# Kernel tuning notes

Measured on AMD Instinct MI355X. Metric: run time of the kernel, lower is better.

Reference implementation:

```python
import jax, jax.numpy as jnp
import numpy as np

B, S, D, H, RANK, NC = 2, 2048, 1024, 16, 128, 16
DH = D // H


def setup_inputs() -> dict:
    key = jax.random.key(0)
    ks = jax.random.split(key, 10)
    x = jax.random.normal(ks[0], (B, S, D), jnp.float32)
    # causal mask, broadcast over batch and heads like torch's [B,1,S,S]
    mask = jnp.tril(jnp.ones((S, S), dtype=bool))[None, None]
    # orthogonal-ish init approximated by scaled gaussian
    compress_neurons = jax.random.normal(ks[1], (NC, D, RANK), jnp.float32) / np.sqrt(D)
    router_Q = jax.random.normal(ks[2], (NC, D), jnp.float32) * 0.02
    router_K = jax.random.normal(ks[3], (NC, D), jnp.float32) * 0.02
    router_V = jax.random.normal(ks[4], (NC, D), jnp.float32) * 0.02
    wQ = jax.random.normal(ks[5], (D, RANK), jnp.float32) / np.sqrt(RANK)
    wK = jax.random.normal(ks[6], (D, RANK), jnp.float32) / np.sqrt(RANK)
    wV = jax.random.normal(ks[7], (D, RANK), jnp.float32) / np.sqrt(RANK)
    wO = jax.random.normal(ks[8], (D, D), jnp.float32) / np.sqrt(D)
    return {"x": x, "mask": mask, "compress_neurons": compress_neurons,
            "router_Q": router_Q, "router_K": router_K, "router_V": router_V,
            "wQ": wQ, "wK": wK, "wV": wV, "wO": wO}


def reference(x, mask, compress_neurons, router_Q, router_K, router_V, wQ, wK, wV, wO):
    def compress(router_w):
        # router scores -> softmax over all n_compress neurons
        w = jax.nn.softmax(jnp.einsum('bsd,nd->bsn', x, router_w), axis=-1)  # [B,S,NC]
        # softmax-weighted sum of all neuron projections (fused einsum)
        return jnp.einsum('bsd,ndr,bsn->bsr', x, compress_neurons, w)  # [B,S,RANK]

    hQ = compress(router_Q)
    hK = compress(router_K)
    hV = compress(router_V)
    # expand rank -> d_model (Linear weight [D,RANK]), then split heads
    Q = jnp.einsum('bsr,dr->bsd', hQ, wQ).reshape(B, S, H, DH).transpose(0, 2, 1, 3)
    K = jnp.einsum('bsr,dr->bsd', hK, wK).reshape(B, S, H, DH).transpose(0, 2, 1, 3)
    V = jnp.einsum('bsr,dr->bsd', hV, wV).reshape(B, S, H, DH).transpose(0, 2, 1, 3)
    scores = jnp.einsum('bhqd,bhkd->bhqk', Q, K) / np.sqrt(DH)  # [B,H,S,S]
    scores = jnp.where(mask, scores, -jnp.inf)
    attn = jax.nn.softmax(scores, axis=-1)
    attn_out = jnp.einsum('bhqk,bhkd->bhqd', attn, V)
    attn_out = attn_out.transpose(0, 2, 1, 3).reshape(B, S, D)
    # dropout omitted (eval mode / dropout=0)
    return jnp.einsum('bsd,ed->bse', attn_out, wO)
```

## Files before the change

kernel.cpp:

```cpp
#include <hip/hip_runtime.h>
#include <hip/hip_bf16.h>
#include <math.h>

#define B_ 2
#define S_ 2048
#define D_ 1024
#define H_ 16
#define RANK_ 128
#define NC_ 16
#define DH_ 64
#define T_ (B_*S_)
#define NZ_ 2176

typedef __attribute__((ext_vector_type(8))) __bf16 bf16x8;
typedef __attribute__((ext_vector_type(8))) unsigned short u16x8;
typedef __attribute__((ext_vector_type(4))) unsigned short u16x4;
typedef __attribute__((ext_vector_type(4))) float f32x4;
typedef __attribute__((ext_vector_type(16))) float f32x16;

#if __has_builtin(__builtin_amdgcn_exp2f)
#define EXP2F(x) __builtin_amdgcn_exp2f(x)
#else
#define EXP2F(x) exp2f(x)
#endif

__device__ __forceinline__ unsigned short f2bu(float f) {
    __hip_bfloat16 h = __float2bfloat16(f);
    unsigned short u; __builtin_memcpy(&u, &h, 2); return u;
}
__device__ __forceinline__ float bu2f(unsigned short u) {
    __hip_bfloat16 h; __builtin_memcpy(&h, &u, 2); return __bfloat162float(h);
}

__device__ __forceinline__ void gl_lds16(const unsigned short* g, unsigned short* l) {
    __builtin_amdgcn_global_load_lds(
        (const __attribute__((address_space(1))) void*)g,
        (__attribute__((address_space(3))) void*)l, 16, 0, 0);
}

__device__ __forceinline__ unsigned cvtpk_bf16(float lo, float hi) {
    unsigned r;
    asm("v_cvt_pk_bf16_f32 %0, %1, %2" : "=v"(r) : "v"(lo), "v"(hi));
    return r;
}
__device__ __forceinline__ void plswap(unsigned &a, unsigned &b) {
    asm("v_permlane32_swap_b32 %0, %1" : "+v"(a), "+v"(b));
}

__device__ __forceinline__ bool sniff_f32(const unsigned* __restrict__ p) {
    int votes = 0;
    #pragma unroll
    for (int i = 0; i < 64; i++) {
        unsigned e = (p[i] >> 23) & 0xFFu;
        votes += (e >= 0x60u && e <= 0x8Fu) ? 1 : 0;
    }
    return votes >= 32;
}

struct Cvt { const void* src[9]; unsigned short* dst[9]; const void* C; unsigned short* Ct; };

__global__ __launch_bounds__(256) void k_inputs(Cvt cv,
    const unsigned* __restrict__ probe)
{
    bool f32 = sniff_f32(probe);
    if (blockIdx.x < 512) {
        int bid = blockIdx.x;
        int d0 = (bid & 15) * 64, r0 = ((bid >> 4) & 1) * 64, n = bid >> 5;
        __shared__ unsigned short tile[64][65];
        for (int idx = threadIdx.x; idx < 4096; idx += 256) {
            int row = idx >> 6, col = idx & 63;
            size_t si = ((size_t)n*D_ + d0 + row)*RANK_ + r0 + col;
            tile[row][col] = f32 ? f2bu(((const float*)cv.C)[si])
                                 : ((const unsigned short*)cv.C)[si];
        }
        __syncthreads();
        for (int idx = threadIdx.x; idx < 4096; idx += 256) {
            int row = idx >> 6, col = idx & 63;
            cv.Ct[((size_t)(n*RANK_ + r0 + row))*D_ + d0 + col] = tile[col][row];
        }
        return;
    }
    const int offs[9] = {0, 4194304, 4210688, 4227072, 4243456,
                         4259840, 4390912, 4521984, 4653056};
    const int total4 = 5701632 / 4;
    int nconv = gridDim.x - 512;
    int stride = nconv * 256;
    for (int g = (blockIdx.x - 512) * 256 + threadIdx.x; g < total4; g += stride) {
        int i = g * 4;
        int seg = 0;
        #pragma unroll
        for (int s = 1; s < 9; s++) seg += (i >= offs[s]) ? 1 : 0;
        int local = i - offs[seg];
        const void* sp = cv.src[seg];
        u16x4 v = {0, 0, 0, 0};
        if (sp) {
            if (f32) {
                f32x4 x = *(const f32x4*)((const float*)sp + local);
                #pragma unroll
                for (int j = 0; j < 4; j++) v[j] = f2bu(x[j]);
            } else {
                v = *(const u16x4*)((const unsigned short*)sp + local);
            }
        }
        *(u16x4*)(cv.dst[seg] + local) = v;
    }
}

template<int MT, int MODE>
__global__ __launch_bounds__(256) void k_mfma_gemm(const unsigned short* __restrict__ A,
    const unsigned short* __restrict__ Bm, void* __restrict__ Cout,
    const unsigned* __restrict__ probe, int M, int N, int K)
{
    bool f32out = false;
    if (MODE == 2) f32out = sniff_f32(probe);
    __shared__ __align__(16) unsigned short As[MT*32*32];
    __shared__ __align__(16) unsigned short Bs[128*32];
    const int tid = threadIdx.x;
    const int wv = tid >> 6, lane = tid & 63;
    const int wm = (wv >> 1) * (MT*16), wn = (wv & 1) * 64;
    const int quad = lane >> 4, l16 = lane & 15;
    const int m0 = blockIdx.x * (MT*32), n0 = blockIdx.y * 128;

    const f32x4 z4 = {0.f, 0.f, 0.f, 0.f};
    f32x4 acc[MT][4];
    #pragma unroll
    for (int i = 0; i < MT; i++)
        #pragma unroll
        for (int j = 0; j < 4; j++) acc[i][j] = z4;

    for (int k0 = 0; k0 < K; k0 += 32) {
        __syncthreads();
        #pragma unroll
        for (int c = 0; c < MT/2; c++) {
            int idx = wv*64 + c*256 + lane;
            gl_lds16(A + (size_t)(m0 + (idx >> 2))*K + k0 + (idx & 3)*8,
                     &As[(wv*64 + c*256)*8]);
        }
        #pragma unroll
        for (int c = 0; c < 2; c++) {
            int idx = wv*64 + c*256 + lane;
            gl_lds16(Bm + (size_t)(n0 + (idx >> 2))*K + k0 + (idx & 3)*8,
                     &Bs[(wv*64 + c*256)*8]);
        }
        __syncthreads();
        bf16x8 af[MT], bfr[4];
        #pragma unroll
        for (int mt = 0; mt < MT; mt++) af[mt]  = *(const bf16x8*)&As[(wm + mt*16 + l16)*32 + quad*8];
        #pragma unroll
        for (int nt = 0; nt < 4; nt++) bfr[nt] = *(const bf16x8*)&Bs[(wn + nt*16 + l16)*32 + quad*8];
        #pragma unroll
        for (int mt = 0; mt < MT; mt++)
            #pragma unroll
            for (int nt = 0; nt < 4; nt++)
                acc[mt][nt] = __builtin_amdgcn_mfma_f32_16x16x32_bf16(af[mt], bfr[nt], acc[mt][nt], 0, 0, 0);
    }
    #pragma unroll
    for (int mt = 0; mt < MT; mt++)
        #pragma unroll
        for (int nt = 0; nt < 4; nt++) {
            int col = n0 + wn + nt*16 + l16;
            #pragma unroll
            for (int r = 0; r < 4; r++) {
                int rowg = m0 + wm + mt*16 + quad*4 + r;
                float v = acc[mt][nt][r];
                if (MODE == 2 && f32out) ((float*)Cout)[(size_t)rowg*N + col] = v;
                else  ((unsigned short*)Cout)[(size_t)rowg*N + col] = f2bu(v);
            }
        }
}

__global__ __launch_bounds__(256) void k_qkv2(const unsigned short* __restrict__ h3,
    const unsigned short* __restrict__ wqkv, unsigned short* __restrict__ QKb,
    unsigned short* __restrict__ Vtg)
{
    __shared__ __align__(16) unsigned short As[128*32];
    __shared__ __align__(16) unsigned short Bs[128*32];
    const int tid = threadIdx.x;
    const int wv = tid >> 6, lane = tid & 63;
    const int wm = (wv >> 1) * 64, wn = (wv & 1) * 64;
    const int quad = lane >> 4, l16 = lane & 15;

    const bool vt = (blockIdx.x >= 512);
    int m0, n0;
    const unsigned short *A, *Bm;
    float scale = 1.f;
    if (!vt) {
        int id = blockIdx.x;
        m0 = (id & 31) * 128;
        n0 = (id >> 5) * 128;
        int w = n0 >> 10;
        A  = h3 + (size_t)w * T_ * RANK_ + (size_t)m0 * RANK_;
        Bm = wqkv + (size_t)w * D_ * RANK_ + (size_t)(n0 & 1023) * RANK_;
        if (w == 0) scale = 0.125f * 1.44269504f;
    } else {
        int id = blockIdx.x - 512;
        m0 = (id & 7) * 128;
        n0 = (id >> 3) * 128;
        A  = wqkv + (size_t)2 * D_ * RANK_ + (size_t)m0 * RANK_;
        Bm = h3 + (size_t)2 * T_ * RANK_ + (size_t)n0 * RANK_;
    }

    const f32x4 z4 = {0.f, 0.f, 0.f, 0.f};
    f32x4 acc[4][4];
    #pragma unroll
    for (int i = 0; i < 4; i++)
        #pragma unroll
        for (int j = 0; j < 4; j++) acc[i][j] = z4;

    for (int k0 = 0; k0 < RANK_; k0 += 32) {
        __syncthreads();
        #pragma unroll
        for (int c = 0; c < 2; c++) {
            int idx = wv*64 + c*256 + lane;
            gl_lds16(A  + (size_t)(idx >> 2)*RANK_ + k0 + (idx & 3)*8,
                     &As[(wv*64 + c*256)*8]);
            gl_lds16(Bm + (size_t)(idx >> 2)*RANK_ + k0 + (idx & 3)*8,
                     &Bs[(wv*64 + c*256)*8]);
        }
        __syncthreads();
        bf16x8 af[4], bfr[4];
        #pragma unroll
        for (int mt = 0; mt < 4; mt++) af[mt]  = *(const bf16x8*)&As[(wm + mt*16 + l16)*32 + quad*8];
        #pragma unroll
        for (int nt = 0; nt < 4; nt++) bfr[nt] = *(const bf16x8*)&Bs[(wn + nt*16 + l16)*32 + quad*8];
        #pragma unroll
        for (int mt = 0; mt < 4; mt++)
            #pragma unroll
            for (int nt = 0; nt < 4; nt++)
                acc[mt][nt] = __builtin_amdgcn_mfma_f32_16x16x32_bf16(af[mt], bfr[nt], acc[mt][nt], 0, 0, 0);
    }
    #pragma unroll
    for (int mt = 0; mt < 4; mt++)
        #pragma unroll
        for (int nt = 0; nt < 4; nt++) {
            #pragma unroll
            for (int r = 0; r < 4; r++) {
                int rowg = m0 + wm + mt*16 + quad*4 + r;
                int col  = n0 + wn + nt*16 + l16;
                float v = acc[mt][nt][r] * scale;
                if (!vt) {
                    QKb[(size_t)(col >> 10)*T_*D_ + (size_t)rowg*D_ + (col & 1023)]
                        = f2bu(v);
                } else {
                    size_t vrow = (size_t)((col >> 11)*H_ + (rowg >> 6))*64 + (rowg & 63);
                    Vtg[vrow*S_ + (col & 2047)] = f2bu(v);
                }
            }
        }
}

__global__ __launch_bounds__(256) void k_hreduce(const unsigned short* __restrict__ z,
    unsigned short* __restrict__ h)
{
    int t0 = blockIdx.x * 2;
    int tg = threadIdx.x >> 7, r = threadIdx.x & 127;
    int t = t0 + tg;
    __shared__ float sc[2][48];
    __shared__ float wl[2][3][16];
    if (threadIdx.x < 96) {
        int tk = threadIdx.x / 48, j = threadIdx.x % 48;
        sc[tk][j] = bu2f(z[(size_t)(t0 + tk)*NZ_ + 2048 + j]);
    }
    __syncthreads();
    if (threadIdx.x < 6) {
        int tk = threadIdx.x / 3, w = threadIdx.x % 3;
        float m = -INFINITY;
        for (int n = 0; n < 16; n++) m = fmaxf(m, sc[tk][w*16 + n]);
        float s = 0.f, e[16];
        for (int n = 0; n < 16; n++) { e[n] = __expf(sc[tk][w*16 + n] - m); s += e[n]; }
        float inv = 1.f / s;
        for (int n = 0; n < 16; n++) wl[tk][w][n] = e[n] * inv;
    }
    __syncthreads();
    const unsigned short* zr = z + (size_t)t * NZ_;
    float acc[3] = {0.f, 0.f, 0.f};
    #pragma unroll
    for (int n = 0; n < NC_; n++) {
        float zv = bu2f(zr[n*RANK_ + r]);
        #pragma unroll
        for (int w = 0; w < 3; w++) acc[w] += wl[tg][w][n] * zv;
    }
    #pragma unroll
    for (int w = 0; w < 3; w++) h[((size_t)w*T_ + t)*RANK_ + r] = f2bu(acc[w]);
}

__global__ __launch_bounds__(256, 2) void k_flash_mfma(const unsigned short* __restrict__ Qm,
    const unsigned short* __restrict__ Km, const unsigned short* __restrict__ Vtg,
    unsigned short* __restrict__ Om)
{
    const int i = blockIdx.x;
    const int half = i >> 8, r_ = i & 255;
    const int gr = r_ & 31, ts = r_ >> 5;
    const int qt = half ? ts : (15 - ts);
    const int hh = gr & 15, b = gr >> 4;

    __shared__ __align__(16) unsigned short Ks[2][64*64];
    __shared__ __align__(16) unsigned short Vs[2][64*64];
    const int tid = threadIdx.x;
    const int w = tid >> 6, lane = tid & 63;
    const int l32 = lane & 31, hi = lane >> 5;
    const size_t base  = ((size_t)b * S_) * D_ + (size_t)hh * DH_;
    const size_t vbase = (size_t)((b*H_ + hh) * 64) * S_;
    const int tokg = qt*128 + w*32 + l32;

    bf16x8 aq[4];
    #pragma unroll
    for (int ks = 0; ks < 4; ks++)
        aq[ks] = *(const bf16x8*)(Qm + base + (size_t)tokg*D_ + ks*16 + hi*8);

    f32x16 oacc[2];
    #pragma unroll
    for (int db = 0; db < 2; db++)
        #pragma unroll
        for (int ii = 0; ii < 16; ii++) oacc[db][ii] = 0.f;
    float lsum = 0.f;

    const int nkt = 2*(qt + 1);

    #pragma unroll
    for (int c = 0; c < 2; c++) {
        int idx = c*256 + tid;
        int row = idx >> 3, j = (idx & 7) ^ (row & 7);
        gl_lds16(Km + base + (size_t)row*D_ + j*8, &Ks[0][(c*256 + (w<<6))*8]);
    }
    #pragma unroll
    for (int c = 0; c < 2; c++) {
        int idx = c*256 + tid;
        int row = idx >> 3, j = (idx & 7) ^ (row & 7);
        gl_lds16(Vtg + vbase + (size_t)row*S_ + j*8, &Vs[0][(c*256 + (w<<6))*8]);
    }

    for (int kt = 0; kt < nkt; kt++) {
        const int cur = kt & 1;
        __syncthreads();

        if (kt + 1 < nkt) {
            #pragma unroll
            for (int c = 0; c < 2; c++) {
                int idx = c*256 + tid;
                int row = idx >> 3, j = (idx & 7) ^ (row & 7);
                gl_lds16(Km + base + (size_t)((kt+1)*64 + row)*D_ + j*8,
                         &Ks[1-cur][(c*256 + (w<<6))*8]);
            }
            #pragma unroll
            for (int c = 0; c < 2; c++) {
                int idx = c*256 + tid;
                int row = idx >> 3, j = (idx & 7) ^ (row & 7);
                gl_lds16(Vtg + vbase + (size_t)row*S_ + (kt+1)*64 + j*8,
                         &Vs[1-cur][(c*256 + (w<<6))*8]);
            }
        }

        f32x16 sacc[2];
        #pragma unroll
        for (int kb = 0; kb < 2; kb++)
            #pragma unroll
            for (int ii = 0; ii < 16; ii++) sacc[kb][ii] = 0.f;
        __builtin_amdgcn_s_setprio(1);
        #pragma unroll
        for (int ks = 0; ks < 4; ks++)
            #pragma unroll
            for (int kb = 0; kb < 2; kb++) {
                int row = kb*32 + l32;
                int c = (ks*2 + hi) ^ (row & 7);
                bf16x8 ak = *(const bf16x8*)&Ks[cur][row*64 + c*8];
                sacc[kb] = __builtin_amdgcn_mfma_f32_32x32x16_bf16(ak, aq[ks], sacc[kb], 0, 0, 0);
            }
        __builtin_amdgcn_s_setprio(0);

        if (kt >= 2*qt) {
            #pragma unroll
            for (int kb = 0; kb < 2; kb++)
                #pragma unroll
                for (int r = 0; r < 16; r++) {
                    int keyg = kt*64 + kb*32 + (r&3) + 8*(r>>2) + 4*hi;
                    if (keyg > tokg) sacc[kb][r] = -INFINITY;
                }
        }

        bf16x8 pa[4];
        #pragma unroll
        for (int kb = 0; kb < 2; kb++) {
            float pv[16];
            #pragma unroll
            for (int r = 0; r < 16; r++) {
                pv[r] = EXP2F(sacc[kb][r]);
                lsum += pv[r];
            }
            unsigned wd[8];
            #pragma unroll
            for (int j = 0; j < 8; j++) wd[j] = cvtpk_bf16(pv[2*j], pv[2*j+1]);
            plswap(wd[0], wd[2]); plswap(wd[1], wd[3]);
            plswap(wd[4], wd[6]); plswap(wd[5], wd[7]);
            union { unsigned u[4]; bf16x8 v; } u0, u1;
            u0.u[0]=wd[0]; u0.u[1]=wd[1]; u0.u[2]=wd[2]; u0.u[3]=wd[3];
            u1.u[0]=wd[4]; u1.u[1]=wd[5]; u1.u[2]=wd[6]; u1.u[3]=wd[7];
            pa[2*kb]   = u0.v;
            pa[2*kb+1] = u1.v;
        }

        __builtin_amdgcn_s_setprio(1);
        #pragma unroll
        for (int ks = 0; ks < 4; ks++)
            #pragma unroll
            for (int db = 0; db < 2; db++) {
                int row = db*32 + l32;
                int c = (ks*2 + hi) ^ (row & 7);
                bf16x8 bv = *(const bf16x8*)&Vs[cur][row*64 + c*8];
                oacc[db] = __builtin_amdgcn_mfma_f32_32x32x16_bf16(pa[ks], bv, oacc[db], 0, 0, 0);
            }
        __builtin_amdgcn_s_setprio(0);
    }

    float l = lsum + __shfl_xor(lsum, 32);
    float inv = 1.f / l;
    #pragma unroll
    for (int r = 0; r < 16; r++) {
        int crow = (r&3) + 8*(r>>2) + 4*hi;
        float invr = __shfl(inv, crow);
        size_t rowo = base + (size_t)(qt*128 + w*32 + crow)*D_;
        #pragma unroll
        for (int db = 0; db < 2; db++)
            Om[rowo + db*32 + l32] = f2bu(oacc[db][r] * invr);
    }
}

extern "C" void kernel_launch(void* const* d_in, const int* in_sizes, int n_in,
                              void* d_out, int out_size, void* d_ws, size_t ws_size,
                              hipStream_t stream)
{
    const unsigned* probe = (const unsigned*)d_in[0];

    unsigned short* u = (unsigned short*)d_ws;
    unsigned short* xc   = u;               size_t o = (size_t)T_*D_;
    unsigned short* wqkv = u + o;           o += (size_t)3*D_*RANK_;
    unsigned short* wOc  = u + o;           o += (size_t)D_*D_;
    unsigned short* Ct   = u + o;           o += (size_t)NZ_*D_;
    unsigned short* h3   = u + o;           o += (size_t)3*T_*RANK_;
    unsigned short* QKb  = u + o;           o += (size_t)2*T_*D_;
    unsigned short* Vtg  = u + o;           o += (size_t)T_*D_;
    unsigned short* z    = u + o;           o += (size_t)T_*NZ_;
    unsigned short* attnb= u + o;           o += (size_t)T_*D_;

    unsigned short* Rp = Ct + (size_t)2048*D_;
    unsigned short* Qb = QKb;
    unsigned short* Kb = QKb + (size_t)T_*D_;

    Cvt cv;
    cv.src[0] = d_in[0]; cv.dst[0] = xc;
    cv.src[1] = d_in[3]; cv.dst[1] = Rp;
    cv.src[2] = d_in[4]; cv.dst[2] = Rp + 16384;
    cv.src[3] = d_in[5]; cv.dst[3] = Rp + 32768;
    cv.src[4] = nullptr; cv.dst[4] = Rp + 49152;
    cv.src[5] = d_in[6]; cv.dst[5] = wqkv;
    cv.src[6] = d_in[7]; cv.dst[6] = wqkv + 131072;
    cv.src[7] = d_in[8]; cv.dst[7] = wqkv + 262144;
    cv.src[8] = d_in[9]; cv.dst[8] = wOc;
    cv.C = d_in[2]; cv.Ct = Ct;
    k_inputs<<<512 + 1024, 256, 0, stream>>>(cv, probe);

    k_mfma_gemm<4,0><<<dim3(T_/128, NZ_/128), 256, 0, stream>>>(
        xc, Ct, z, nullptr, T_, NZ_, D_);

    k_hreduce<<<T_/2, 256, 0, stream>>>(z, h3);

    k_qkv2<<<768, 256, 0, stream>>>(h3, wqkv, QKb, Vtg);

    k_flash_mfma<<<dim3(512), 256, 0, stream>>>(Qb, Kb, Vtg, attnb);

    k_mfma_gemm<2,2><<<dim3(T_/64, D_/128), 256, 0, stream>>>(
        attnb, wOc, d_out, probe, T_, D_, D_);
}
```

Baseline: 216.2 us.

## Triple-buffer K/V tiles and software-pipeline QK^T one tile ahead

```diff
diff --git a/kernel.cpp b/kernel.cpp
--- a/kernel.cpp
+++ b/kernel.cpp
@@ -294,8 +294,8 @@
     const int qt = half ? ts : (15 - ts);
     const int hh = gr & 15, b = gr >> 4;
 
-    __shared__ __align__(16) unsigned short Ks[2][64*64];
-    __shared__ __align__(16) unsigned short Vs[2][64*64];
+    __shared__ __align__(16) unsigned short Ks[3][64*64];
+    __shared__ __align__(16) unsigned short Vs[3][64*64];
     const int tid = threadIdx.x;
     const int w = tid >> 6, lane = tid & 63;
     const int l32 = lane & 31, hi = lane >> 5;
@@ -317,65 +317,60 @@
 
     const int nkt = 2*(qt + 1);
 
-    #pragma unroll
-    for (int c = 0; c < 2; c++) {
-        int idx = c*256 + tid;
-        int row = idx >> 3, j = (idx & 7) ^ (row & 7);
-        gl_lds16(Km + base + (size_t)row*D_ + j*8, &Ks[0][(c*256 + (w<<6))*8]);
-    }
-    #pragma unroll
-    for (int c = 0; c < 2; c++) {
-        int idx = c*256 + tid;
-        int row = idx >> 3, j = (idx & 7) ^ (row & 7);
-        gl_lds16(Vtg + vbase + (size_t)row*S_ + j*8, &Vs[0][(c*256 + (w<<6))*8]);
-    }
+    auto STAGE = [&](int kt_, int bf_) {
+        #pragma unroll
+        for (int c = 0; c < 2; c++) {
+            int idx = c*256 + tid;
+            int row = idx >> 3, j = (idx & 7) ^ (row & 7);
+            gl_lds16(Km + base + (size_t)(kt_*64 + row)*D_ + j*8,
+                     &Ks[bf_][(c*256 + (w<<6))*8]);
+        }
+        #pragma unroll
+        for (int c = 0; c < 2; c++) {
+            int idx = c*256 + tid;
+            int row = idx >> 3, j = (idx & 7) ^ (row & 7);
+            gl_lds16(Vtg + vbase + (size_t)row*S_ + kt_*64 + j*8,
+                     &Vs[bf_][(c*256 + (w<<6))*8]);
+        }
+    };
+
+    auto QKT = [&](int bf_, f32x16& s0, f32x16& s1) {
+        #pragma unroll
+        for (int ii = 0; ii < 16; ii++) { s0[ii] = 0.f; s1[ii] = 0.f; }
+        const unsigned short* Kp = Ks[bf_];
+        #pragma unroll
+        for (int ks = 0; ks < 4; ks++) {
+            int c0 = (ks*2 + hi) ^ (l32 & 7);
+            bf16x8 ak0 = *(const bf16x8*)&Kp[l32*64 + c0*8];
+            s0 = __builtin_amdgcn_mfma_f32_32x32x16_bf16(ak0, aq[ks], s0, 0, 0, 0);
+            int row1 = 32 + l32;
+            int c1 = (ks*2 + hi) ^ (row1 & 7);
+            bf16x8 ak1 = *(const bf16x8*)&Kp[row1*64 + c1*8];
+            s1 = __builtin_amdgcn_mfma_f32_32x32x16_bf16(ak1, aq[ks], s1, 0, 0, 0);
+        }
+    };
+
+    STAGE(0, 0);
+    STAGE(1, 1);
+    __syncthreads();
+
+    f32x16 sA0, sA1, sB0, sB1;
+    QKT(0, sA0, sA1);
 
     for (int kt = 0; kt < nkt; kt++) {
-        const int cur = kt & 1;
-        __syncthreads();
-
-        if (kt + 1 < nkt) {
-            #pragma unroll
-            for (int c = 0; c < 2; c++) {
-                int idx = c*256 + tid;
-                int row = idx >> 3, j = (idx & 7) ^ (row & 7);
-                gl_lds16(Km + base + (size_t)((kt+1)*64 + row)*D_ + j*8,
-                         &Ks[1-cur][(c*256 + (w<<6))*8]);
-            }
-            #pragma unroll
-            for (int c = 0; c < 2; c++) {
-                int idx = c*256 + tid;
-                int row = idx >> 3, j = (idx & 7) ^ (row & 7);
-                gl_lds16(Vtg + vbase + (size_t)row*S_ + (kt+1)*64 + j*8,
-                         &Vs[1-cur][(c*256 + (w<<6))*8]);
-            }
-        }
-
-        f32x16 sacc[2];
-        #pragma unroll
-        for (int kb = 0; kb < 2; kb++)
-            #pragma unroll
-            for (int ii = 0; ii < 16; ii++) sacc[kb][ii] = 0.f;
-        __builtin_amdgcn_s_setprio(1);
-        #pragma unroll
-        for (int ks = 0; ks < 4; ks++)
-            #pragma unroll
-            for (int kb = 0; kb < 2; kb++) {
-                int row = kb*32 + l32;
-                int c = (ks*2 + hi) ^ (row & 7);
-                bf16x8 ak = *(const bf16x8*)&Ks[cur][row*64 + c*8];
-                sacc[kb] = __builtin_amdgcn_mfma_f32_32x32x16_bf16(ak, aq[ks], sacc[kb], 0, 0, 0);
-            }
-        __builtin_amdgcn_s_setprio(0);
+        const int cur = kt % 3;
+        if (kt + 2 < nkt) STAGE(kt + 2, (kt + 2) % 3);
+        if (kt + 1 < nkt) QKT((kt + 1) % 3, sB0, sB1);
 
         if (kt >= 2*qt) {
             #pragma unroll
-            for (int kb = 0; kb < 2; kb++)
-                #pragma unroll
-                for (int r = 0; r < 16; r++) {
-                    int keyg = kt*64 + kb*32 + (r&3) + 8*(r>>2) + 4*hi;
-                    if (keyg > tokg) sacc[kb][r] = -INFINITY;
-                }
+            for (int r = 0; r < 16; r++) {
+                int crow = (r&3) + 8*(r>>2) + 4*hi;
+                int keyg0 = kt*64 + crow;
+                int keyg1 = kt*64 + 32 + crow;
+                if (keyg0 > tokg) sA0[r] = -INFINITY;
+                if (keyg1 > tokg) sA1[r] = -INFINITY;
+            }
         }
 
         bf16x8 pa[4];
@@ -384,7 +379,7 @@
             float pv[16];
             #pragma unroll
             for (int r = 0; r < 16; r++) {
-                pv[r] = EXP2F(sacc[kb][r]);
+                pv[r] = EXP2F(kb ? sA1[r] : sA0[r]);
                 lsum += pv[r];
             }
             unsigned wd[8];
@@ -399,7 +394,6 @@
             pa[2*kb+1] = u1.v;
         }
 
-        __builtin_amdgcn_s_setprio(1);
         #pragma unroll
         for (int ks = 0; ks < 4; ks++)
             #pragma unroll
@@ -409,7 +403,9 @@
                 bf16x8 bv = *(const bf16x8*)&Vs[cur][row*64 + c*8];
                 oacc[db] = __builtin_amdgcn_mfma_f32_32x32x16_bf16(pa[ks], bv, oacc[db], 0, 0, 0);
             }
-        __builtin_amdgcn_s_setprio(0);
+
+        if (kt + 1 < nkt) { sA0 = sB0; sA1 = sB1; }
+        __syncthreads();
     }
 
     float l = lsum + __shfl_xor(lsum, 32);
```

Result: no change. 215.2 us (-0.5%).
